# Performance work log

Hardware: AMD Instinct MI355X
Metric: run time of the kernel (lower is better)

## Reference

```python
import jax, jax.numpy as jnp
import numpy as np

NUM_LAYERS = 2
SHAPES = [(100, 100), (50, 50), (25, 25), (13, 13)]  # (H, W) per level
D, NH, NP, NL = 256, 8, 4, 4
DH = D // NH
DFF = 1024
B = 2
S = sum(h * w for h, w in SHAPES)  # 13294


def layer_norm(x, g, b, eps=1e-5):
    m = x.mean(-1, keepdims=True)
    v = jnp.var(x, axis=-1, keepdims=True)
    return (x - m) * jax.lax.rsqrt(v + eps) * g + b


def get_reference_points(valid_ratios):
    refs = []
    for lvl, (H_, W_) in enumerate(SHAPES):
        ry, rx = jnp.meshgrid(jnp.linspace(0.5, H_ - 0.5, H_),
                              jnp.linspace(0.5, W_ - 0.5, W_), indexing='ij')
        ry = ry.reshape(-1)[None] / (valid_ratios[:, None, lvl, 1] * H_)
        rx = rx.reshape(-1)[None] / (valid_ratios[:, None, lvl, 0] * W_)
        refs.append(jnp.stack([rx, ry], -1))
    ref = jnp.concatenate(refs, 1)                      # [B, S, 2]
    return ref[:, :, None] * valid_ratios[:, None]      # [B, S, NL, 2]


def sample_level(value_l, H_, W_, loc):
    # value_l: [B, nH, H*W, Dh]; loc: [B, Q, nH, P, 2] normalized in [0,1]
    x = loc[..., 0] * W_ - 0.5
    y = loc[..., 1] * H_ - 0.5
    x0 = jnp.floor(x)
    y0 = jnp.floor(y)
    Bq, Q = loc.shape[0], loc.shape[1]
    acc = 0.
    corners = ((x0, y0, (x0 + 1 - x) * (y0 + 1 - y)),
               (x0 + 1, y0, (x - x0) * (y0 + 1 - y)),
               (x0, y0 + 1, (x0 + 1 - x) * (y - y0)),
               (x0 + 1, y0 + 1, (x - x0) * (y - y0)))
    for xi, yi, w in corners:  # zero-padding grid_sample: invalid corners contribute 0
        valid = (xi >= 0) & (xi <= W_ - 1) & (yi >= 0) & (yi <= H_ - 1)
        idx = (jnp.clip(yi, 0, H_ - 1) * W_ + jnp.clip(xi, 0, W_ - 1)).astype(jnp.int32)
        idx = jnp.transpose(idx, (0, 2, 1, 3)).reshape(Bq, NH, Q * NP)
        g = jnp.take_along_axis(value_l, idx[..., None], axis=2)  # [B,nH,Q*P,Dh]
        wv = jnp.transpose((w * valid).astype(value_l.dtype), (0, 2, 1, 3)).reshape(Bq, NH, Q * NP)
        acc = acc + g * wv[..., None]
    return acc.reshape(Bq, NH, Q, NP, DH)


def msda(query, ref, src, W_val, b_val, W_off, b_off, W_attn, b_attn, W_out, b_out):
    Bq, Q = query.shape[:2]
    value = (src @ W_val + b_val).reshape(Bq, S, NH, DH)
    off = (query @ W_off + b_off).reshape(Bq, Q, NH, NL, NP, 2)
    attn = jax.nn.softmax((query @ W_attn + b_attn).reshape(Bq, Q, NH, NL * NP), -1)
    attn = attn.reshape(Bq, Q, NH, NL, NP)
    normalizer = jnp.array([[w, h] for h, w in SHAPES], dtype=query.dtype)  # [NL,2] (x,y)
    loc = ref[:, :, None, :, None, :] + off / normalizer[None, None, None, :, None, :]
    out = jnp.zeros((Bq, NH, Q, DH), query.dtype)
    start = 0
    for l, (H_, W_) in enumerate(SHAPES):
        v_l = jnp.transpose(value[:, start:start + H_ * W_], (0, 2, 1, 3))  # [B,nH,HW,Dh]
        samp = sample_level(v_l, H_, W_, loc[:, :, :, l])                    # [B,nH,Q,P,Dh]
        w_l = jnp.transpose(attn[:, :, :, l], (0, 2, 1, 3))                  # [B,nH,Q,P]
        out = out + (samp * w_l[..., None]).sum(3)
        start += H_ * W_
    out = jnp.transpose(out, (0, 2, 1, 3)).reshape(Bq, Q, D)
    return out @ W_out + b_out


def setup_inputs() -> dict:
    key = jax.random.key(0)
    ks = jax.random.split(key, 12)
    sc = 0.02
    inp = {
        'src': jax.random.normal(ks[0], (B, S, D), jnp.float32),
        'spatial_shapes': np.array(SHAPES, dtype=np.int64),
        'valid_ratios': jnp.ones((B, NL, 2), jnp.float32),
        'W_off': sc * jax.random.normal(ks[1], (NUM_LAYERS, D, NH * NL * NP * 2), jnp.float32),
        'b_off': jnp.zeros((NUM_LAYERS, NH * NL * NP * 2), jnp.float32),
        'W_attn': sc * jax.random.normal(ks[2], (NUM_LAYERS, D, NH * NL * NP), jnp.float32),
        'b_attn': jnp.zeros((NUM_LAYERS, NH * NL * NP), jnp.float32),
        'W_val': sc * jax.random.normal(ks[3], (NUM_LAYERS, D, D), jnp.float32),
        'b_val': jnp.zeros((NUM_LAYERS, D), jnp.float32),
        'W_out': sc * jax.random.normal(ks[4], (NUM_LAYERS, D, D), jnp.float32),
        'b_out': jnp.zeros((NUM_LAYERS, D), jnp.float32),
        'ln1_g': jnp.ones((NUM_LAYERS, D), jnp.float32),
        'ln1_b': jnp.zeros((NUM_LAYERS, D), jnp.float32),
        'W1': sc * jax.random.normal(ks[5], (NUM_LAYERS, D, DFF), jnp.float32),
        'b1': jnp.zeros((NUM_LAYERS, DFF), jnp.float32),
        'W2': sc * jax.random.normal(ks[6], (NUM_LAYERS, DFF, D), jnp.float32),
        'b2': jnp.zeros((NUM_LAYERS, D), jnp.float32),
        'ln2_g': jnp.ones((NUM_LAYERS, D), jnp.float32),
        'ln2_b': jnp.zeros((NUM_LAYERS, D), jnp.float32),
    }
    return inp


def reference(src, spatial_shapes, valid_ratios, W_off, b_off, W_attn, b_attn,
              W_val, b_val, W_out, b_out, ln1_g, ln1_b, W1, b1, W2, b2, ln2_g, ln2_b):
    # Deformable-DETR encoder stack (dropout=0 / eval mode, pos=None, no padding mask).
    ref = get_reference_points(valid_ratios)  # [B, S, NL, 2]
    x = src
    for i in range(NUM_LAYERS):
        x2 = msda(x, ref, x, W_val[i], b_val[i], W_off[i], b_off[i],
                  W_attn[i], b_attn[i], W_out[i], b_out[i])
        x = layer_norm(x + x2, ln1_g[i], ln1_b[i])
        h = jax.nn.relu(x @ W1[i] + b1[i]) @ W2[i] + b2[i]
        x = layer_norm(x + h, ln2_g[i], ln2_b[i])
    return x
```

## Files before the change

### kernel.cpp

```cpp
#include <hip/hip_runtime.h>
#include <math.h>


#define S_TOT 13294
#define BATCH 2
#define M_TOT (BATCH * S_TOT)
#define M_PAD 26624

typedef __attribute__((ext_vector_type(8))) short short8;
typedef __attribute__((ext_vector_type(4))) float floatx4;
typedef __attribute__((ext_vector_type(2))) float floatx2;

#define AS1C(p) ((const __attribute__((address_space(1))) void*)(p))
#define AS3(p)  ((__attribute__((address_space(3))) void*)(p))

static __device__ __forceinline__ unsigned short f2bf(float x) {
    union { float f; unsigned u; } v; v.f = x;
    unsigned r = v.u + 0x7FFFu + ((v.u >> 16) & 1u);
    return (unsigned short)(r >> 16);
}
static __device__ __forceinline__ float b2f(unsigned short u) {
    union { unsigned u; float f; } v; v.u = (unsigned)u << 16; return v.f;
}
static __device__ __forceinline__ float bflo(unsigned u) {
    union { unsigned u; float f; } v; v.u = u << 16; return v.f;
}
static __device__ __forceinline__ float bfhi(unsigned u) {
    union { unsigned u; float f; } v; v.u = u & 0xFFFF0000u; return v.f;
}
static __device__ __forceinline__ float braw(unsigned u) {
    union { unsigned u; float f; } v; v.u = u; return v.f;
}

template<int TM, bool RELU, bool BF16OUT, bool PROJ, bool SUM>
__global__ __launch_bounds__(256)
void mgemm(const unsigned short* __restrict__ A,
           const unsigned short* __restrict__ BT,
           const float* __restrict__ bias,
           const float* __restrict__ bias2,
           const float* __restrict__ bias3,
           const unsigned short* __restrict__ R,
           unsigned short* __restrict__ Cb,
           unsigned short* __restrict__ Cb2,
           int nbmPer,
           int M, int N, int K)
{
    constexpr int WM = (TM == 128) ? 2 : 1;
    constexpr int WN = 4 / WM;
    constexpr int MI = TM / (WM * 16);
    constexpr int NI = 128 / (WN * 16);
    __shared__ __align__(16) unsigned short smemA[2 * TM * 32];
    __shared__ __align__(16) unsigned short smemB[2 * 128 * 32];
    const int tid  = threadIdx.x;
    const int lane = tid & 63;
    const int w    = tid >> 6;
    const int wm   = w % WM, wn = w / WM;
    const int lr   = lane & 15, quad = lane >> 4;
    const int id  = blockIdx.x;
    const int x8  = id & 7;
    const int k9  = id >> 3;
    const int bm  = (x8 * nbmPer + (k9 % nbmPer)) * TM;
    const int bn  = (k9 / nbmPer) * 128;

    floatx4 acc[MI][NI];
    #pragma unroll
    for (int i = 0; i < MI; ++i)
        #pragma unroll
        for (int j = 0; j < NI; ++j)
            acc[i][j] = (floatx4){0.f, 0.f, 0.f, 0.f};

    const int srow = lane >> 2;
    const int selt = (lane & 3) << 3;

    for (int k0 = 0; k0 < K; k0 += 64) {
        #pragma unroll
        for (int c = 0; c < 2; ++c) {
            if (TM == 128) {
                #pragma unroll
                for (int jj = 0; jj < 2; ++jj) {
                    const int j = 2 * w + jj;
                    const unsigned short* ga = A  + (size_t)(bm + j * 16 + srow) * K + k0 + c * 32 + selt;
                    const unsigned short* gb = BT + (size_t)(bn + j * 16 + srow) * K + k0 + c * 32 + selt;
                    __builtin_amdgcn_global_load_lds(AS1C(ga), AS3(smemA + c * (TM * 32) + j * 512), 16, 0, 0);
                    __builtin_amdgcn_global_load_lds(AS1C(gb), AS3(smemB + c * 4096 + j * 512), 16, 0, 0);
                }
            } else {
                const unsigned short* ga = A + (size_t)(bm + w * 16 + srow) * K + k0 + c * 32 + selt;
                __builtin_amdgcn_global_load_lds(AS1C(ga), AS3(smemA + c * (TM * 32) + w * 512), 16, 0, 0);
                #pragma unroll
                for (int jj = 0; jj < 2; ++jj) {
                    const int j = 2 * w + jj;
                    const unsigned short* gb = BT + (size_t)(bn + j * 16 + srow) * K + k0 + c * 32 + selt;
                    __builtin_amdgcn_global_load_lds(AS1C(gb), AS3(smemB + c * 4096 + j * 512), 16, 0, 0);
                }
            }
        }
        __syncthreads();

        #pragma unroll
        for (int c = 0; c < 2; ++c) {
            short8 av[MI], bv[NI];
            #pragma unroll
            for (int mi = 0; mi < MI; ++mi)
                av[mi] = *(const short8*)&smemA[c * (TM * 32) + (wm * MI * 16 + mi * 16 + lr) * 32 + quad * 8];
            #pragma unroll
            for (int ni = 0; ni < NI; ++ni)
                bv[ni] = *(const short8*)&smemB[c * 4096 + (wn * NI * 16 + ni * 16 + lr) * 32 + quad * 8];
            #pragma unroll
            for (int mi = 0; mi < MI; ++mi)
                #pragma unroll
                for (int ni = 0; ni < NI; ++ni)
                    acc[mi][ni] = __builtin_amdgcn_mfma_f32_16x16x32_bf16(
                        av[mi], bv[ni], acc[mi][ni], 0, 0, 0);
        }
        __syncthreads();
    }

    #pragma unroll
    for (int mi = 0; mi < MI; ++mi) {
        #pragma unroll
        for (int ni = 0; ni < NI; ++ni) {
            #pragma unroll
            for (int r = 0; r < 4; ++r) {
                const int row = bm + wm * MI * 16 + mi * 16 + quad * 4 + r;
                const int col = bn + wn * NI * 16 + ni * 16 + lr;
                if (PROJ) {
                    const float bb = (col < 256) ? bias[col]
                                   : (col < 512) ? bias2[col - 256]
                                                 : bias3[col - 512];
                    const float v = acc[mi][ni][r] + bb;
                    if (col < 256) Cb[(size_t)row * 256 + col] = f2bf(v);
                    else           Cb2[(size_t)row * 384 + (col - 256)] = f2bf(v);
                } else if (SUM) {
                    const float v = acc[mi][ni][r] + bias[col]
                                  + b2f(R[(size_t)row * 256 + col]);
                    Cb[(size_t)row * 256 + col] = f2bf(v);
                } else {
                    float v = acc[mi][ni][r] + bias[col];
                    if (RELU) v = fmaxf(v, 0.0f);
                    if (BF16OUT) Cb[(size_t)row * N + col] = f2bf(v);
                }
            }
        }
    }
}

template<bool HASF, bool HASB>
__global__ __launch_bounds__(256)
void ln_kernel(const unsigned short* __restrict__ S,
               const float* __restrict__ g, const float* __restrict__ beta,
               float* __restrict__ outF, unsigned short* __restrict__ outB,
               int M)
{
    const int lane = threadIdx.x & 63;
    const int row  = blockIdx.x * 4 + (threadIdx.x >> 6);
    if (row >= M) return;
    const int c4 = lane * 4;
    const uint2 sv = *(const uint2*)(S + (size_t)row * 256 + c4);
    const float x0 = bflo(sv.x);
    const float x1 = bfhi(sv.x);
    const float x2 = bflo(sv.y);
    const float x3 = bfhi(sv.y);
    float p = (x0 + x1) + (x2 + x3);
    float q = (x0 * x0 + x1 * x1) + (x2 * x2 + x3 * x3);
    #pragma unroll
    for (int o = 1; o < 64; o <<= 1) {
        p += __shfl_xor(p, o, 64);
        q += __shfl_xor(q, o, 64);
    }
    const float mean = p * (1.0f / 256.0f);
    const float var  = q * (1.0f / 256.0f) - mean * mean;
    const float rs   = rsqrtf(var + 1e-5f);
    const float4 gv = *(const float4*)(g + c4);
    const float4 bv = *(const float4*)(beta + c4);
    const float y0 = (x0 - mean) * rs * gv.x + bv.x;
    const float y1 = (x1 - mean) * rs * gv.y + bv.y;
    const float y2 = (x2 - mean) * rs * gv.z + bv.z;
    const float y3 = (x3 - mean) * rs * gv.w + bv.w;
    if (HASF) {
        float4 o4; o4.x = y0; o4.y = y1; o4.z = y2; o4.w = y3;
        *(float4*)(outF + (size_t)row * 256 + c4) = o4;
    }
    if (HASB) {
        uint2 o2;
        o2.x = (unsigned)f2bf(y0) | ((unsigned)f2bf(y1) << 16);
        o2.y = (unsigned)f2bf(y2) | ((unsigned)f2bf(y3) << 16);
        *(uint2*)(outB + (size_t)row * 256 + c4) = o2;
    }
}

__global__ __launch_bounds__(256)
void convpad(const float* __restrict__ X, unsigned short* __restrict__ Y, int M)
{
    const int idx = blockIdx.x * 256 + threadIdx.x;
    const int row = idx >> 6;
    const int c4  = (idx & 63) << 2;
    if (row >= M_PAD) return;
    float4 v = {0.f, 0.f, 0.f, 0.f};
    if (row < M) v = ((const float4*)(X + (size_t)row * 256))[c4 >> 2];
    unsigned p0 = (unsigned)f2bf(v.x) | ((unsigned)f2bf(v.y) << 16);
    unsigned p1 = (unsigned)f2bf(v.z) | ((unsigned)f2bf(v.w) << 16);
    uint2 o; o.x = p0; o.y = p1;
    *(uint2*)(Y + (size_t)row * 256 + c4) = o;
}

struct WJobs {
    const float* W[12];
    unsigned short* WT[12];
    int K[12], N[12], tx[12], start[12];
};

__global__ __launch_bounds__(256)
void wtrans_all(WJobs jb)
{
    __shared__ float t[32][33];
    const int bx = blockIdx.x;
    int seg = 0;
    #pragma unroll
    for (int s = 1; s < 12; ++s) if (bx >= jb.start[s]) seg = s;
    const float* W = jb.W[seg];
    unsigned short* WT = jb.WT[seg];
    const int K = jb.K[seg], N = jb.N[seg], tx = jb.tx[seg];
    const int local = bx - jb.start[seg];
    const int n0 = (local % tx) * 32, k0 = (local / tx) * 32;
    const int c = threadIdx.x & 31, r0 = threadIdx.x >> 5;
    #pragma unroll
    for (int rr = r0; rr < 32; rr += 8)
        t[rr][c] = W[(size_t)(k0 + rr) * N + n0 + c];
    __syncthreads();
    #pragma unroll
    for (int rr = r0; rr < 32; rr += 8)
        WT[(size_t)(n0 + rr) * K + k0 + c] = f2bf(t[c][rr]);
}

__global__ __launch_bounds__(256)
void msda_kernel(const unsigned short* __restrict__ valb,
                 const unsigned short* __restrict__ oab,
                 const float* __restrict__ vr,
                 unsigned short* __restrict__ out)
{
    __shared__ __align__(16) char smeta[8 * 128 * 32];
    const int t = threadIdx.x;
    const int bid = (blockIdx.x & 7) * 416 + (blockIdx.x >> 3);

    {
        const int wv = t >> 6, lane = t & 63;
        const int lqA = wv * 2 + (lane >> 5);
        const int bq = bid * 8 + lqA;
        const int h = (lane >> 2) & 7;
        const int j = lane & 3;
        if (bq < M_TOT) {
            const int b = (bq >= S_TOT) ? 1 : 0;
            const int q = bq - b * S_TOT;
            const int bofs = b * (S_TOT * 512);
            int Hq, rr, cc, lq;
            if (q < 10000)      { lq = 0; Hq = 100; rr = q / 100;              cc = q - rr * 100; }
            else if (q < 12500) { lq = 1; Hq = 50;  int r2 = q - 10000; rr = r2 / 50; cc = r2 - rr * 50; }
            else if (q < 13125) { lq = 2; Hq = 25;  int r2 = q - 12500; rr = r2 / 25; cc = r2 - rr * 25; }
            else                { lq = 3; Hq = 13;  int r2 = q - 13125; rr = r2 / 13; cc = r2 - rr * 13; }
            const float rxb = (cc + 0.5f) / (vr[(b * 4 + lq) * 2 + 0] * (float)Hq);
            const float ryb = (rr + 0.5f) / (vr[(b * 4 + lq) * 2 + 1] * (float)Hq);
            const int HWt[4] = {100, 50, 25, 13};
            const int stt[4] = {0, 10000, 12500, 13125};
            const int HW = HWt[j], st = stt[j];
            const float fW = (float)HW;
            const float refxw = rxb * vr[(b * 4 + j) * 2 + 0] * fW - 0.5f;
            const float refyw = ryb * vr[(b * 4 + j) * 2 + 1] * fW - 0.5f;
            const unsigned short* row = oab + (size_t)bq * 384;
            const uint2 lgu = *(const uint2*)(row + 256 + h * 16 + j * 4);
            const float l0 = bflo(lgu.x), l1 = bfhi(lgu.x);
            const float l2 = bflo(lgu.y), l3 = bfhi(lgu.y);
            float mx = fmaxf(fmaxf(l0, l1), fmaxf(l2, l3));
            mx = fmaxf(mx, __shfl_xor(mx, 1, 64));
            mx = fmaxf(mx, __shfl_xor(mx, 2, 64));
            const float e0 = __expf(l0 - mx), e1 = __expf(l1 - mx);
            const float e2 = __expf(l2 - mx), e3 = __expf(l3 - mx);
            float ss = e0 + e1 + e2 + e3;
            ss += __shfl_xor(ss, 1, 64);
            ss += __shfl_xor(ss, 2, 64);
            const float inv = 1.0f / ss;
            const uint4 ou = *(const uint4*)(row + h * 32 + j * 8);
            const float oxs[4] = {bflo(ou.x), bflo(ou.y), bflo(ou.z), bflo(ou.w)};
            const float oys[4] = {bfhi(ou.x), bfhi(ou.y), bfhi(ou.z), bfhi(ou.w)};
            const float aw[4]  = {e0 * inv, e1 * inv, e2 * inv, e3 * inv};
            char* mb = smeta + (size_t)(lqA * 128 + h * 16 + j * 4) * 32;
            const int swz = ((h * 4 + j) & 7) << 4;
            #pragma unroll
            for (int p = 0; p < 4; ++p) {
                const float x = refxw + oxs[p];
                const float y = refyw + oys[p];
                const float x0f = floorf(x), y0f = floorf(y);
                const int x0 = (int)x0f, y0 = (int)y0f;
                const float fx = x - x0f, fy = y - y0f;
                const float wb[4] = {(1.f - fx) * (1.f - fy), fx * (1.f - fy),
                                     (1.f - fx) * fy,         fx * fy};
                const int xs[2] = {x0, x0 + 1};
                const int ys2[2] = {y0, y0 + 1};
                int iv[4]; float wv4[4];
                #pragma unroll
                for (int k = 0; k < 4; ++k) {
                    const int xi = xs[k & 1], yi = ys2[k >> 1];
                    const bool vld = ((unsigned)xi < (unsigned)HW) && ((unsigned)yi < (unsigned)HW);
                    const int xc = min(max(xi, 0), HW - 1);
                    const int yc = min(max(yi, 0), HW - 1);
                    iv[k] = bofs + ((st + yc * HW + xc) << 9) + (h << 6);
                    wv4[k] = vld ? wb[k] * aw[p] : 0.0f;
                }
                int4 i4; i4.x = iv[0]; i4.y = iv[1]; i4.z = iv[2]; i4.w = iv[3];
                float4 w4; w4.x = wv4[0]; w4.y = wv4[1]; w4.z = wv4[2]; w4.w = wv4[3];
                *(int4*)(mb + ((p * 32) ^ swz)) = i4;
                *(float4*)(mb + ((p * 32 + 16) ^ swz)) = w4;
            }
        }
    }
    __syncthreads();
    {
        const int lq2 = t >> 5;
        const int r = t & 31;
        const int h2 = r >> 2;
        const int cg = r & 3;
        const int bq2 = bid * 8 + lq2;
        if (bq2 < M_TOT) {
            const char* vbase = (const char*)valb;
            const unsigned cgo = cg * 16;
            floatx2 a0 = {0.f, 0.f}, a1 = {0.f, 0.f}, a2 = {0.f, 0.f}, a3 = {0.f, 0.f};
            const char* mb2 = smeta + (size_t)(lq2 * 128 + h2 * 16) * 32;
            #pragma unroll 4
            for (int s = 0; s < 16; ++s) {
                const int swz2 = ((h2 * 4 + (s >> 2)) & 7) << 4;
                const int4  iv = *(const int4*)(mb2 + ((s * 32) ^ swz2));
                const float4 w4 = *(const float4*)(mb2 + ((s * 32 + 16) ^ swz2));
                const uint4 u0 = *(const uint4*)(vbase + (unsigned)(iv.x + cgo));
                const uint4 u1 = *(const uint4*)(vbase + (unsigned)(iv.y + cgo));
                const uint4 u2 = *(const uint4*)(vbase + (unsigned)(iv.z + cgo));
                const uint4 u3 = *(const uint4*)(vbase + (unsigned)(iv.w + cgo));
                #define ACC8(UU, WW) { \
                    const floatx2 w2 = {WW, WW}; \
                    const floatx2 t0 = {bflo(UU.x), braw(UU.x)}; \
                    const floatx2 t1 = {bflo(UU.y), braw(UU.y)}; \
                    const floatx2 t2 = {bflo(UU.z), braw(UU.z)}; \
                    const floatx2 t3 = {bflo(UU.w), braw(UU.w)}; \
                    a0 += w2 * t0; a1 += w2 * t1; a2 += w2 * t2; a3 += w2 * t3; }
                ACC8(u0, w4.x) ACC8(u1, w4.y) ACC8(u2, w4.z) ACC8(u3, w4.w)
                #undef ACC8
            }
            uint4 o;
            o.x = (unsigned)f2bf(a0.x) | ((unsigned)f2bf(a0.y) << 16);
            o.y = (unsigned)f2bf(a1.x) | ((unsigned)f2bf(a1.y) << 16);
            o.z = (unsigned)f2bf(a2.x) | ((unsigned)f2bf(a2.y) << 16);
            o.w = (unsigned)f2bf(a3.x) | ((unsigned)f2bf(a3.y) << 16);
            *(uint4*)(out + (size_t)bq2 * 256 + h2 * 32 + cg * 8) = o;
        }
    }
}

extern "C" void kernel_launch(void* const* d_in, const int* in_sizes, int n_in,
                              void* d_out, int out_size, void* d_ws, size_t ws_size,
                              hipStream_t stream)
{
    const float* src    = (const float*)d_in[0];
    const float* vr     = (const float*)d_in[2];
    const float* W_off  = (const float*)d_in[3];
    const float* b_off  = (const float*)d_in[4];
    const float* W_attn = (const float*)d_in[5];
    const float* b_attn = (const float*)d_in[6];
    const float* W_val  = (const float*)d_in[7];
    const float* b_val  = (const float*)d_in[8];
    const float* W_out  = (const float*)d_in[9];
    const float* b_out  = (const float*)d_in[10];
    const float* ln1_g  = (const float*)d_in[11];
    const float* ln1_b  = (const float*)d_in[12];
    const float* W1     = (const float*)d_in[13];
    const float* b1     = (const float*)d_in[14];
    const float* W2     = (const float*)d_in[15];
    const float* b2     = (const float*)d_in[16];
    const float* ln2_g  = (const float*)d_in[17];
    const float* ln2_b  = (const float*)d_in[18];
    float* out = (float*)d_out;

    const int M = M_TOT;

    char* wsb = (char*)d_ws;
    unsigned short* HBF  = (unsigned short*)wsb;
    unsigned short* OAB  = (unsigned short*)wsb;
    unsigned short* VALB = (unsigned short*)(wsb + 20447232);
    unsigned short* S1   = (unsigned short*)wsb;
    unsigned short* X1B  = (unsigned short*)(wsb + 54525952);
    unsigned short* S2   = (unsigned short*)(wsb + 68157440);
    unsigned short* RB   = (unsigned short*)(wsb + 81788928);
    unsigned short* YBF  = (unsigned short*)(wsb + 95420416);
    unsigned short* WT   = (unsigned short*)(wsb + 109051904);

    const size_t LWT = 753664;
    const size_t oProj = 0, oOut = 163840, oW1 = 229376, oW2 = 491520;

    WJobs jb;
    int startAcc = 0;
    for (int i = 0; i < 2; ++i) {
        unsigned short* wt = WT + i * LWT;
        const float* srcs[6] = {W_val + i * 65536, W_off + i * 65536, W_attn + i * 32768,
                                W_out + i * 65536, W1 + i * 262144, W2 + i * 262144};
        unsigned short* dsts[6] = {wt + oProj, wt + oProj + 65536, wt + oProj + 131072,
                                   wt + oOut, wt + oW1, wt + oW2};
        const int Ks[6] = {256, 256, 256, 256, 256, 1024};
        const int Ns[6] = {256, 256, 128, 256, 1024, 256};
        for (int s = 0; s < 6; ++s) {
            const int idx = i * 6 + s;
            jb.W[idx] = srcs[s]; jb.WT[idx] = dsts[s];
            jb.K[idx] = Ks[s]; jb.N[idx] = Ns[s]; jb.tx[idx] = Ns[s] / 32;
            jb.start[idx] = startAcc;
            startAcc += (Ns[s] / 32) * (Ks[s] / 32);
        }
    }
    wtrans_all<<<dim3(startAcc), 256, 0, stream>>>(jb);

    const int GM128 = M_PAD / 128;
    const int GM64  = M_PAD / 64;
    const int GLN   = M_TOT / 4;
    const dim3 blk(256);

    for (int i = 0; i < 2; ++i) {
        unsigned short* wt = WT + i * LWT;

        if (i == 0)
            convpad<<<dim3(M_PAD / 4), blk, 0, stream>>>(src, RB, M);

        mgemm<64, false, false, true, false><<<dim3(5 * GM64), blk, 0, stream>>>(
            RB, wt + oProj, b_val + i * 256, b_off + i * 256, b_attn + i * 128,
            nullptr, VALB, OAB, GM64 / 8, M, 640, 256);

        msda_kernel<<<dim3(3328), blk, 0, stream>>>(VALB, OAB, vr, YBF);

        mgemm<64, false, false, false, true><<<dim3(2 * GM64), blk, 0, stream>>>(
            YBF, wt + oOut, b_out + i * 256, nullptr, nullptr,
            RB, S1, nullptr, GM64 / 8, M, 256, 256);

        ln_kernel<false, true><<<dim3(GLN), blk, 0, stream>>>(
            S1, ln1_g + i * 256, ln1_b + i * 256, nullptr, X1B, M);

        mgemm<128, true, true, false, false><<<dim3(8 * GM128), blk, 0, stream>>>(
            X1B, wt + oW1, b1 + i * 1024, nullptr, nullptr,
            nullptr, HBF, nullptr, GM128 / 8, M, 1024, 256);

        mgemm<64, false, false, false, true><<<dim3(2 * GM64), blk, 0, stream>>>(
            HBF, wt + oW2, b2 + i * 256, nullptr, nullptr,
            X1B, S2, nullptr, GM64 / 8, M, 256, 1024);

        if (i == 0)
            ln_kernel<false, true><<<dim3(GLN), blk, 0, stream>>>(
                S2, ln2_g + i * 256, ln2_b + i * 256, nullptr, RB, M);
        else
            ln_kernel<true, false><<<dim3(GLN), blk, 0, stream>>>(
                S2, ln2_g + i * 256, ln2_b + i * 256, out, nullptr, M);
    }
}
```

Before: 394.7 us.

## Double-buffer GEMM LDS tiles with async prefetch two stages ahead

The GEMM main loop now keeps two LDS buffers per operand. It issues global-to-LDS loads for tile k+2 while tile k is computed, with explicit vmcnt waits and raw barriers replacing the full syncthreads. The goal is to hide global load latency behind MFMA work. In exchange it doubles LDS use per block, which may cut occupancy, and the hand-counted vmcnt values must match the number of loads issued per stage.

```diff
diff --git a/kernel.cpp b/kernel.cpp
--- a/kernel.cpp
+++ b/kernel.cpp
@@ -49,8 +49,9 @@
     constexpr int WN = 4 / WM;
     constexpr int MI = TM / (WM * 16);
     constexpr int NI = 128 / (WN * 16);
-    __shared__ __align__(16) unsigned short smemA[2 * TM * 32];
-    __shared__ __align__(16) unsigned short smemB[2 * 128 * 32];
+    constexpr int ABUF = TM * 64;
+    __shared__ __align__(16) unsigned short smemA[2 * ABUF];
+    __shared__ __align__(16) unsigned short smemB[2 * 8192];
     const int tid  = threadIdx.x;
     const int lane = tid & 63;
     const int w    = tid >> 6;
@@ -72,7 +73,8 @@
     const int srow = lane >> 2;
     const int selt = (lane & 3) << 3;
 
-    for (int k0 = 0; k0 < K; k0 += 64) {
+    auto stage = [&](int kt, int buf) {
+        const int k0 = kt << 6;
         #pragma unroll
         for (int c = 0; c < 2; ++c) {
             if (TM == 128) {
@@ -81,31 +83,44 @@
                     const int j = 2 * w + jj;
                     const unsigned short* ga = A  + (size_t)(bm + j * 16 + srow) * K + k0 + c * 32 + selt;
                     const unsigned short* gb = BT + (size_t)(bn + j * 16 + srow) * K + k0 + c * 32 + selt;
-                    __builtin_amdgcn_global_load_lds(AS1C(ga), AS3(smemA + c * (TM * 32) + j * 512), 16, 0, 0);
-                    __builtin_amdgcn_global_load_lds(AS1C(gb), AS3(smemB + c * 4096 + j * 512), 16, 0, 0);
+                    __builtin_amdgcn_global_load_lds(AS1C(ga), AS3(smemA + buf * ABUF + c * (TM * 32) + j * 512), 16, 0, 0);
+                    __builtin_amdgcn_global_load_lds(AS1C(gb), AS3(smemB + buf * 8192 + c * 4096 + j * 512), 16, 0, 0);
                 }
             } else {
                 const unsigned short* ga = A + (size_t)(bm + w * 16 + srow) * K + k0 + c * 32 + selt;
-                __builtin_amdgcn_global_load_lds(AS1C(ga), AS3(smemA + c * (TM * 32) + w * 512), 16, 0, 0);
+                __builtin_amdgcn_global_load_lds(AS1C(ga), AS3(smemA + buf * ABUF + c * (TM * 32) + w * 512), 16, 0, 0);
                 #pragma unroll
                 for (int jj = 0; jj < 2; ++jj) {
                     const int j = 2 * w + jj;
                     const unsigned short* gb = BT + (size_t)(bn + j * 16 + srow) * K + k0 + c * 32 + selt;
-                    __builtin_amdgcn_global_load_lds(AS1C(gb), AS3(smemB + c * 4096 + j * 512), 16, 0, 0);
+                    __builtin_amdgcn_global_load_lds(AS1C(gb), AS3(smemB + buf * 8192 + c * 4096 + j * 512), 16, 0, 0);
                 }
             }
         }
-        __syncthreads();
+    };
+
+    const int NK = K >> 6;
+    stage(0, 0);
+    stage(1, 1);
+    for (int kt = 0; kt < NK; ++kt) {
+        const int buf = kt & 1;
+        if (kt + 1 < NK) {
+            if (TM == 128) asm volatile("s_waitcnt vmcnt(8)" ::: "memory");
+            else           asm volatile("s_waitcnt vmcnt(6)" ::: "memory");
+        } else {
+            asm volatile("s_waitcnt vmcnt(0)" ::: "memory");
+        }
+        __builtin_amdgcn_s_barrier();
 
         #pragma unroll
         for (int c = 0; c < 2; ++c) {
             short8 av[MI], bv[NI];
             #pragma unroll
             for (int mi = 0; mi < MI; ++mi)
-                av[mi] = *(const short8*)&smemA[c * (TM * 32) + (wm * MI * 16 + mi * 16 + lr) * 32 + quad * 8];
+                av[mi] = *(const short8*)&smemA[buf * ABUF + c * (TM * 32) + (wm * MI * 16 + mi * 16 + lr) * 32 + quad * 8];
             #pragma unroll
             for (int ni = 0; ni < NI; ++ni)
-                bv[ni] = *(const short8*)&smemB[c * 4096 + (wn * NI * 16 + ni * 16 + lr) * 32 + quad * 8];
+                bv[ni] = *(const short8*)&smemB[buf * 8192 + c * 4096 + (wn * NI * 16 + ni * 16 + lr) * 32 + quad * 8];
             #pragma unroll
             for (int mi = 0; mi < MI; ++mi)
                 #pragma unroll
@@ -113,7 +128,9 @@
                     acc[mi][ni] = __builtin_amdgcn_mfma_f32_16x16x32_bf16(
                         av[mi], bv[ni], acc[mi][ni], 0, 0, 0);
         }
-        __syncthreads();
+        asm volatile("s_waitcnt lgkmcnt(0)" ::: "memory");
+        __builtin_amdgcn_s_barrier();
+        if (kt + 2 < NK) stage(kt + 2, buf);
     }
 
     #pragma unroll
```

After: 404.9 us. 1.03x slower.
